# Performance work log

Hardware: AMD Instinct MI355X
Metric: run time of the kernel (lower is better)

The kernel has to match this reference:

```python
import jax, jax.numpy as jnp
import numpy as np


def setup_inputs() -> dict:
    key = jax.random.key(0)
    k1, k2 = jax.random.split(key)
    hw, bs, c = 16384, 16, 256
    nq = 100
    return {
        "query_feat": jax.random.normal(k1, (hw, bs, c), dtype=jnp.float32),
        "support_feat": jax.random.normal(k2, (nq, bs, c), dtype=jnp.float32),
        "h": 128,
        "w": 128,
    }


def reference(query_feat, support_feat, h, w):
    # query_feat: [hw, bs, c], support_feat: [nq, bs, c]
    hw, bs, c = query_feat.shape
    nq = support_feat.shape[0]
    dtype = query_feat.dtype

    side_normalizer = jnp.array([w, h], dtype=dtype)[None, None, :]  # [1,1,2]

    q = jnp.transpose(query_feat, (1, 0, 2))    # [bs, hw, c]
    s = jnp.transpose(support_feat, (1, 0, 2))  # [bs, nq, c]

    # bmm(q, s^T) -> [bs, hw, nq]; transpose -> [bs, nq, hw]
    similarity_flat = jnp.einsum('bnc,bkc->bnk', s, q)        # [bs, nq, hw]
    similarity = similarity_flat.reshape(bs, nq, h, w)

    # coordinate grid: stack([grid_x, grid_y]) with 'ij' meshgrid, flattened to [hw, 2]
    ys = jnp.linspace(0.5, h - 0.5, h, dtype=jnp.float32)
    xs = jnp.linspace(0.5, w - 0.5, w, dtype=jnp.float32)
    grid_y, grid_x = jnp.meshgrid(ys, xs, indexing='ij')      # [h, w] each
    coord = jnp.stack([grid_x, grid_y], axis=-1).reshape(hw, 2)  # [hw, 2]

    similarity_softmax = jax.nn.softmax(similarity_flat, axis=-1)  # [bs, nq, hw]

    proposal_for_loss = jnp.einsum('bnk,kd->bnd', similarity_softmax, coord) / side_normalizer

    # peak masking: argmax -> one_hot -> reshape (w, h) [faithful to original swap] -> 3x3 max pool
    max_pos = jnp.argmax(similarity_flat, axis=-1)            # [bs, nq]
    max_mask = jax.nn.one_hot(max_pos, hw, dtype=jnp.float32).reshape(bs, nq, w, h)
    local_max_mask = jax.lax.reduce_window(
        max_mask, -jnp.inf, jax.lax.max,
        window_dimensions=(1, 1, 3, 3), window_strides=(1, 1, 1, 1),
        padding=((0, 0), (0, 0), (1, 1), (1, 1)),
    ).reshape(bs, nq, hw)                                     # [bs, nq, hw]

    local_sm = similarity_softmax * local_max_mask            # [bs, nq, hw]
    local_sm = local_sm / (jnp.sum(local_sm, axis=-1, keepdims=True) + 1e-10)
    proposals = jnp.einsum('bnk,kd->bnd', local_sm, coord) / side_normalizer

    return (proposal_for_loss, similarity, proposals)
```

## Files before the change

kernel.cpp:

```cpp
#include <hip/hip_runtime.h>
#include <math.h>

#define HW   16384
#define BS   16
#define C    256
#define NQ   100
#define NQP  112
#define Hh   128
#define Ww   128

#define SIM_OFF   3200
#define PROPS_OFF (3200 + 26214400)

#define BM 256
#define BK 32
#define NBLK (HW / BM)

typedef _Float16 half8 __attribute__((ext_vector_type(8)));
typedef float f32x4 __attribute__((ext_vector_type(4)));

__device__ __forceinline__ void gll16(const void* gp, void* lp) {
    __builtin_amdgcn_global_load_lds((const __attribute__((address_space(1))) void*)gp,
                                     (__attribute__((address_space(3))) void*)lp, 16, 0, 0);
}

__device__ __forceinline__ void split8(const float4 a, const float4 b, half8& hi, half8& lo) {
    float f[8] = {a.x, a.y, a.z, a.w, b.x, b.y, b.z, b.w};
    _Float16 h[8], l[8];
    #pragma unroll
    for (int i = 0; i < 8; ++i) {
        h[i] = (_Float16)f[i];
        l[i] = (_Float16)(f[i] - (float)h[i]);
    }
    hi = *(half8*)h;
    lo = *(half8*)l;
}

__global__ __launch_bounds__(256) void split_S_kernel(const float* __restrict__ S,
                                                      _Float16* __restrict__ shi,
                                                      _Float16* __restrict__ slo)
{
    int idx4 = blockIdx.x * 256 + threadIdx.x;
    int idx = idx4 * 4;
    if (idx >= BS * NQP * C) return;
    int b = idx / (NQP * C);
    int rem = idx - b * (NQP * C);
    int n = rem / C;
    int k = rem - n * C;
    float4 v = make_float4(0.f, 0.f, 0.f, 0.f);
    if (n < NQ) v = *(const float4*)(S + ((size_t)n * BS + b) * C + k);
    _Float16 h[4], l[4];
    float f[4] = {v.x, v.y, v.z, v.w};
    #pragma unroll
    for (int i = 0; i < 4; ++i) {
        h[i] = (_Float16)f[i];
        l[i] = (_Float16)(f[i] - (float)h[i]);
    }
    *(uint2*)(shi + idx) = *(uint2*)h;
    *(uint2*)(slo + idx) = *(uint2*)l;
}

template<bool USE_WS>
__global__ __launch_bounds__(256, 2) void gemm_kernel(const float* __restrict__ Q,
                                                      const float* __restrict__ S,
                                                      const _Float16* __restrict__ ShiG,
                                                      const _Float16* __restrict__ SloG,
                                                      float* __restrict__ out,
                                                      float* __restrict__ pm,
                                                      float* __restrict__ pz,
                                                      float* __restrict__ pwx,
                                                      float* __restrict__ pwy,
                                                      int* __restrict__ pidx)
{
    __shared__ __align__(16) float    Qf[BM * BK];
    __shared__ __align__(16) _Float16 SHI[NQP * BK];
    __shared__ __align__(16) _Float16 SLO[NQP * BK];
    __shared__ __align__(16) float Ws[NQP][4][4];

    const int b    = blockIdx.y;
    const int hw0  = blockIdx.x * BM;
    const int t    = threadIdx.x;
    const int wid  = t >> 6;
    const int lane = t & 63;
    const int lr   = lane & 15;
    const int lg   = lane >> 4;

    f32x4 acc[4][7];
    #pragma unroll
    for (int am = 0; am < 4; ++am)
        #pragma unroll
        for (int bn = 0; bn < 7; ++bn)
            acc[am][bn] = (f32x4)(0.f);

    const int q_r8 = lane >> 3;
    const int q_gc = (lane & 7) ^ q_r8;
    const int s_r  = lane >> 2;
    const int s_gc = (lane & 3) ^ ((lane >> 3) & 3);

    for (int k0 = 0; k0 < C; k0 += BK) {
        #pragma unroll
        for (int p = 0; p < 8; ++p) {
            int rt = wid * 64 + p * 8;
            const float* g = Q + ((size_t)(hw0 + rt + q_r8) * BS + b) * C + k0 + q_gc * 4;
            gll16(g, &Qf[rt * BK]);
        }
        if (USE_WS) {
            for (int i = wid; i < 14; i += 4) {
                int r0 = (i % 7) * 16;
                _Float16* dst = (i < 7) ? &SHI[r0 * BK] : &SLO[r0 * BK];
                const _Float16* src = (i < 7) ? ShiG : SloG;
                const _Float16* g = src + ((size_t)b * NQP + r0 + s_r) * C + k0 + s_gc * 8;
                gll16(g, dst);
            }
        }
        __syncthreads();

        half8 qhi[4], qlo[4];
        #pragma unroll
        for (int am = 0; am < 4; ++am) {
            int row = wid * 64 + 16 * am + lr;
            int r7 = row & 7;
            float4 qa = *(const float4*)&Qf[row * BK + (((2 * lg + 0) ^ r7) << 2)];
            float4 qb = *(const float4*)&Qf[row * BK + (((2 * lg + 1) ^ r7) << 2)];
            split8(qa, qb, qhi[am], qlo[am]);
        }

        #pragma unroll
        for (int bn = 0; bn < 7; ++bn) {
            int row = 16 * bn + lr;
            half8 shi, slo;
            if (USE_WS) {
                int slot = lg ^ ((row >> 1) & 3);
                shi = *(const half8*)&SHI[row * BK + slot * 8];
                slo = *(const half8*)&SLO[row * BK + slot * 8];
            } else {
                if (row < NQ) {
                    const float* g = S + ((size_t)row * BS + b) * C + k0 + 8 * lg;
                    float4 sa = *(const float4*)g;
                    float4 sb = *(const float4*)(g + 4);
                    split8(sa, sb, shi, slo);
                } else {
                    shi = (half8)(_Float16)0.f;
                    slo = (half8)(_Float16)0.f;
                }
            }
            #pragma unroll
            for (int am = 0; am < 4; ++am) {
                acc[am][bn] = __builtin_amdgcn_mfma_f32_16x16x32_f16(qhi[am], shi, acc[am][bn], 0, 0, 0);
                acc[am][bn] = __builtin_amdgcn_mfma_f32_16x16x32_f16(qhi[am], slo, acc[am][bn], 0, 0, 0);
                acc[am][bn] = __builtin_amdgcn_mfma_f32_16x16x32_f16(qlo[am], shi, acc[am][bn], 0, 0, 0);
            }
        }
        __syncthreads();
    }

    float* simb = out + SIM_OFF;
    const int hwl0 = wid * 64 + 4 * lg;
    #pragma unroll
    for (int bn = 0; bn < 7; ++bn) {
        int nq = 16 * bn + lr;
        if (nq < NQ) {
            size_t rbase = ((size_t)(b * NQ + nq)) * HW + hw0 + hwl0;
            #pragma unroll
            for (int am = 0; am < 4; ++am)
                *(float4*)&simb[rbase + 16 * am] =
                    make_float4(acc[am][bn][0], acc[am][bn][1], acc[am][bn][2], acc[am][bn][3]);
        }
        if (USE_WS) {
            float vm = acc[0][bn][0];
            int   ci = hw0 + hwl0;
            #pragma unroll
            for (int am = 0; am < 4; ++am)
                #pragma unroll
                for (int j = 0; j < 4; ++j) {
                    float v = acc[am][bn][j];
                    if (v > vm) { vm = v; ci = hw0 + hwl0 + 16 * am + j; }
                }
            float z = 0.f, wx = 0.f;
            #pragma unroll
            for (int am = 0; am < 4; ++am)
                #pragma unroll
                for (int j = 0; j < 4; ++j) {
                    float e = __expf(acc[am][bn][j] - vm);
                    z += e;
                    wx += e * ((float)((hwl0 + 16 * am + j) & 127) + 0.5f);
                }
            #pragma unroll
            for (int off = 16; off < 64; off <<= 1) {
                float om = __shfl_xor(vm, off);
                int   oc = __shfl_xor(ci, off);
                float oz = __shfl_xor(z, off);
                float ox = __shfl_xor(wx, off);
                bool take = (om > vm) || (om == vm && oc < ci);
                float mn = take ? om : vm;
                float ss = __expf(vm - mn);
                float so = __expf(om - mn);
                z  = z * ss + oz * so;
                wx = wx * ss + ox * so;
                vm = mn;
                ci = take ? oc : ci;
            }
            if (lg == 0) {
                Ws[nq][wid][0] = vm;
                Ws[nq][wid][1] = __int_as_float(ci);
                Ws[nq][wid][2] = z;
                Ws[nq][wid][3] = wx;
            }
        }
    }
    if (USE_WS) {
        __syncthreads();
        if (t < NQ) {
            int nq = t;
            float M = -3.4e38f; int gi = 0;
            float mw[4], zw[4], xw[4]; int cw[4];
            #pragma unroll
            for (int w = 0; w < 4; ++w) {
                f32x4 tu = *(const f32x4*)&Ws[nq][w][0];
                mw[w] = tu[0]; cw[w] = __float_as_int(tu[1]); zw[w] = tu[2]; xw[w] = tu[3];
                if (mw[w] > M || (mw[w] == M && cw[w] < gi)) { M = mw[w]; gi = cw[w]; }
            }
            float ybase = (float)(hw0 >> 7) + 0.5f;
            float Zp = 0.f, WXp = 0.f, WYp = 0.f;
            #pragma unroll
            for (int w = 0; w < 4; ++w) {
                float s = __expf(mw[w] - M);
                Zp  += zw[w] * s;
                WXp += xw[w] * s;
                WYp += zw[w] * s * (ybase + (float)(w >> 1));
            }
            size_t pbase = ((size_t)b * NBLK + blockIdx.x) * NQ + nq;
            pm[pbase] = M; pz[pbase] = Zp; pwx[pbase] = WXp; pwy[pbase] = WYp;
            pidx[pbase] = gi;
        }
    }
}

__global__ __launch_bounds__(256) void finalize_kernel(const float* __restrict__ sim,
                                                       const float* __restrict__ pm,
                                                       const float* __restrict__ pz,
                                                       const float* __restrict__ pwx,
                                                       const float* __restrict__ pwy,
                                                       const int* __restrict__ pidx,
                                                       float* __restrict__ out)
{
    const int rglob = blockIdx.x * 4 + (threadIdx.x >> 6);
    const int lane  = threadIdx.x & 63;
    const int b     = rglob / NQ;
    const int n     = rglob - b * NQ;
    const size_t base = ((size_t)b * NBLK + lane) * NQ + n;

    float m  = pm[base];
    float z  = pz[base];
    float wx = pwx[base];
    float wy = pwy[base];
    int   gi = pidx[base];

    float v = m; int vi = gi;
    #pragma unroll
    for (int off = 1; off < 64; off <<= 1) {
        float ov = __shfl_xor(v, off);
        int   oi = __shfl_xor(vi, off);
        if (ov > v || (ov == v && oi < vi)) { v = ov; vi = oi; }
    }
    float s  = __expf(m - v);
    float Z  = z * s;
    float WX = wx * s;
    float WY = wy * s;
    #pragma unroll
    for (int off = 1; off < 64; off <<= 1) {
        Z  += __shfl_xor(Z, off);
        WX += __shfl_xor(WX, off);
        WY += __shfl_xor(WY, off);
    }
    if (lane == 0) {
        out[(size_t)rglob * 2 + 0] = (WX / Z) * (1.f / 128.f);
        out[(size_t)rglob * 2 + 1] = (WY / Z) * (1.f / 128.f);
        const float* srow = sim + (size_t)rglob * HW;
        int pr = vi >> 7, pc = vi & 127;
        float ls = 0.f, lx = 0.f, ly = 0.f;
        #pragma unroll
        for (int dr = -1; dr <= 1; ++dr) {
            #pragma unroll
            for (int dc = -1; dc <= 1; ++dc) {
                int r = pr + dr, c = pc + dc;
                if (r >= 0 && r < Ww && c >= 0 && c < Hh) {
                    int k = r * Hh + c;
                    float e = __expf(srow[k] - v);
                    ls += e;
                    lx += e * ((float)(k & 127) + 0.5f);
                    ly += e * ((float)(k >> 7) + 0.5f);
                }
            }
        }
        float denom = ls + 1e-10f * Z;
        out[PROPS_OFF + (size_t)rglob * 2 + 0] = (lx / denom) * (1.f / 128.f);
        out[PROPS_OFF + (size_t)rglob * 2 + 1] = (ly / denom) * (1.f / 128.f);
    }
}

__global__ __launch_bounds__(256) void reduce_kernel(const float* __restrict__ sim,
                                                     float* __restrict__ out)
{
    __shared__ float rowbuf[HW];
    __shared__ float s_pm[4];
    __shared__ int   s_pi[4];
    __shared__ float s_red[4][3];
    __shared__ float s_gmax;
    __shared__ int   s_gidx;

    const int row = blockIdx.x;
    const int t   = threadIdx.x;
    const int wid  = t >> 6;
    const int lane = t & 63;
    const float4* src4 = (const float4*)(sim + (size_t)row * HW);

    float vmax = -3.4e38f;
    int   vidx = 0;
    #pragma unroll
    for (int p = 0; p < 16; ++p) {
        int i4 = p * 256 + t;
        float4 v = src4[i4];
        *(float4*)&rowbuf[i4 * 4] = v;
        int base = i4 * 4;
        if (v.x > vmax) { vmax = v.x; vidx = base; }
        if (v.y > vmax) { vmax = v.y; vidx = base + 1; }
        if (v.z > vmax) { vmax = v.z; vidx = base + 2; }
        if (v.w > vmax) { vmax = v.w; vidx = base + 3; }
    }
    #pragma unroll
    for (int off = 32; off > 0; off >>= 1) {
        float ov = __shfl_down(vmax, off);
        int   oi = __shfl_down(vidx, off);
        if (ov > vmax || (ov == vmax && oi < vidx)) { vmax = ov; vidx = oi; }
    }
    if (lane == 0) { s_pm[wid] = vmax; s_pi[wid] = vidx; }
    __syncthreads();
    if (t == 0) {
        float gm = s_pm[0]; int gi = s_pi[0];
        #pragma unroll
        for (int wv = 1; wv < 4; ++wv) {
            float ov = s_pm[wv]; int oi = s_pi[wv];
            if (ov > gm || (ov == gm && oi < gi)) { gm = ov; gi = oi; }
        }
        s_gmax = gm; s_gidx = gi;
    }
    __syncthreads();
    const float gmax = s_gmax;

    float z = 0.f, wx = 0.f, wy = 0.f;
    #pragma unroll
    for (int p = 0; p < 16; ++p) {
        int i4 = p * 256 + t;
        float4 v = *(const float4*)&rowbuf[i4 * 4];
        int i = i4 * 4;
        float e0 = __expf(v.x - gmax), e1 = __expf(v.y - gmax);
        float e2 = __expf(v.z - gmax), e3 = __expf(v.w - gmax);
        z += (e0 + e1) + (e2 + e3);
        float cy = (float)(i >> 7) + 0.5f;
        float cx0 = (float)(i & (Ww - 1)) + 0.5f;
        wx += e0 * cx0 + e1 * (cx0 + 1.f) + e2 * (cx0 + 2.f) + e3 * (cx0 + 3.f);
        wy += (e0 + e1 + e2 + e3) * cy;
    }
    #pragma unroll
    for (int off = 32; off > 0; off >>= 1) {
        z  += __shfl_down(z, off);
        wx += __shfl_down(wx, off);
        wy += __shfl_down(wy, off);
    }
    if (lane == 0) { s_red[wid][0] = z; s_red[wid][1] = wx; s_red[wid][2] = wy; }
    __syncthreads();

    if (t == 0) {
        float Z = 0.f, WX = 0.f, WY = 0.f;
        #pragma unroll
        for (int wv = 0; wv < 4; ++wv) { Z += s_red[wv][0]; WX += s_red[wv][1]; WY += s_red[wv][2]; }

        out[(size_t)row * 2 + 0] = (WX / Z) * (1.0f / (float)Ww);
        out[(size_t)row * 2 + 1] = (WY / Z) * (1.0f / (float)Hh);

        int p  = s_gidx;
        int pr = p / Hh;
        int pc = p % Hh;
        float lsum = 0.f, lwx = 0.f, lwy = 0.f;
        #pragma unroll
        for (int di = -1; di <= 1; ++di) {
            #pragma unroll
            for (int dj = -1; dj <= 1; ++dj) {
                int r = pr + di, c = pc + dj;
                if (r >= 0 && r < Ww && c >= 0 && c < Hh) {
                    int k = r * Hh + c;
                    float e = __expf(rowbuf[k] - gmax);
                    lsum += e;
                    lwx  += e * ((float)(k & (Ww - 1)) + 0.5f);
                    lwy  += e * ((float)(k >> 7) + 0.5f);
                }
            }
        }
        float denom = lsum + 1e-10f * Z;
        out[PROPS_OFF + (size_t)row * 2 + 0] = (lwx / denom) * (1.0f / (float)Ww);
        out[PROPS_OFF + (size_t)row * 2 + 1] = (lwy / denom) * (1.0f / (float)Hh);
    }
}

extern "C" void kernel_launch(void* const* d_in, const int* in_sizes, int n_in,
                              void* d_out, int out_size, void* d_ws, size_t ws_size,
                              hipStream_t stream) {
    const float* Q = (const float*)d_in[0];
    const float* S = (const float*)d_in[1];
    float* out = (float*)d_out;

    const size_t splitElems = (size_t)BS * NQP * C;
    const size_t splitBytes = splitElems * 2 * sizeof(_Float16);
    const size_t nPart = (size_t)BS * NQ * NBLK;
    const size_t pOff  = (splitBytes + 255) & ~(size_t)255;
    const size_t wsNeeded = pOff + nPart * 5 * sizeof(float);

    if (ws_size >= wsNeeded) {
        _Float16* shi = (_Float16*)d_ws;
        _Float16* slo = shi + splitElems;
        float* pm  = (float*)((char*)d_ws + pOff);
        float* pz  = pm + nPart;
        float* pwx = pz + nPart;
        float* pwy = pwx + nPart;
        int*   pidx = (int*)(pwy + nPart);
        split_S_kernel<<<dim3((unsigned)((splitElems / 4 + 255) / 256)), 256, 0, stream>>>(S, shi, slo);
        gemm_kernel<true><<<dim3(HW / BM, BS), 256, 0, stream>>>(Q, S, shi, slo, out,
                                                                 pm, pz, pwx, pwy, pidx);
        finalize_kernel<<<dim3(BS * NQ / 4), 256, 0, stream>>>(out + SIM_OFF, pm, pz, pwx, pwy, pidx, out);
    } else {
        gemm_kernel<false><<<dim3(HW / BM, BS), 256, 0, stream>>>(Q, S, nullptr, nullptr, out,
                                                                  nullptr, nullptr, nullptr, nullptr, nullptr);
        reduce_kernel<<<dim3(BS * NQ), 256, 0, stream>>>(out + SIM_OFF, out);
    }
}
```

Baseline: 110.3 us.

## Halve GEMM tile rows, double-buffer Q staging, read split S directly from global

The GEMM tile shrinks from 256 to 128 rows per block with occupancy raised to 3, and Q tiles are double-buffered in LDS so the next K slice loads while MFMAs run. The per-step __syncthreads barriers are removed. The hi/lo split S operands are now read straight from global memory (L2/L1) instead of being staged in LDS. Since each block now covers exactly one image row, the y-weight partial is dropped and recomputed in finalize from the block index, which also handles two partials per lane. Risks include a possible race from removing the barriers between LDS writes and reads, more global traffic for S, and higher register pressure.

```diff
diff --git a/kernel.cpp b/kernel.cpp
--- a/kernel.cpp
+++ b/kernel.cpp
@@ -12,7 +12,7 @@
 #define SIM_OFF   3200
 #define PROPS_OFF (3200 + 26214400)
 
-#define BM 256
+#define BM 128
 #define BK 32
 #define NBLK (HW / BM)
 
@@ -61,7 +61,7 @@
 }
 
 template<bool USE_WS>
-__global__ __launch_bounds__(256, 2) void gemm_kernel(const float* __restrict__ Q,
+__global__ __launch_bounds__(256, 3) void gemm_kernel(const float* __restrict__ Q,
                                                       const float* __restrict__ S,
                                                       const _Float16* __restrict__ ShiG,
                                                       const _Float16* __restrict__ SloG,
@@ -69,12 +69,9 @@
                                                       float* __restrict__ pm,
                                                       float* __restrict__ pz,
                                                       float* __restrict__ pwx,
-                                                      float* __restrict__ pwy,
                                                       int* __restrict__ pidx)
 {
-    __shared__ __align__(16) float    Qf[BM * BK];
-    __shared__ __align__(16) _Float16 SHI[NQP * BK];
-    __shared__ __align__(16) _Float16 SLO[NQP * BK];
+    __shared__ __align__(16) float Qf[2][BM * BK];
     __shared__ __align__(16) float Ws[NQP][4][4];
 
     const int b    = blockIdx.y;
@@ -85,105 +82,105 @@
     const int lr   = lane & 15;
     const int lg   = lane >> 4;
 
-    f32x4 acc[4][7];
-    #pragma unroll
-    for (int am = 0; am < 4; ++am)
+    f32x4 acc[2][7];
+    #pragma unroll
+    for (int am = 0; am < 2; ++am)
         #pragma unroll
         for (int bn = 0; bn < 7; ++bn)
             acc[am][bn] = (f32x4)(0.f);
 
     const int q_r8 = lane >> 3;
     const int q_gc = (lane & 7) ^ q_r8;
-    const int s_r  = lane >> 2;
-    const int s_gc = (lane & 3) ^ ((lane >> 3) & 3);
-
-    for (int k0 = 0; k0 < C; k0 += BK) {
-        #pragma unroll
-        for (int p = 0; p < 8; ++p) {
-            int rt = wid * 64 + p * 8;
+
+    auto stageQ = [&](int buf, int k0) {
+        #pragma unroll
+        for (int p = 0; p < 4; ++p) {
+            int rt = wid * 32 + p * 8;
             const float* g = Q + ((size_t)(hw0 + rt + q_r8) * BS + b) * C + k0 + q_gc * 4;
-            gll16(g, &Qf[rt * BK]);
-        }
-        if (USE_WS) {
-            for (int i = wid; i < 14; i += 4) {
-                int r0 = (i % 7) * 16;
-                _Float16* dst = (i < 7) ? &SHI[r0 * BK] : &SLO[r0 * BK];
-                const _Float16* src = (i < 7) ? ShiG : SloG;
-                const _Float16* g = src + ((size_t)b * NQP + r0 + s_r) * C + k0 + s_gc * 8;
-                gll16(g, dst);
-            }
-        }
-        __syncthreads();
-
-        half8 qhi[4], qlo[4];
-        #pragma unroll
-        for (int am = 0; am < 4; ++am) {
-            int row = wid * 64 + 16 * am + lr;
+            gll16(g, &Qf[buf][rt * BK]);
+        }
+    };
+
+    stageQ(0, 0);
+    #pragma unroll 2
+    for (int step = 0; step < 8; ++step) {
+        const int k0  = step * BK;
+        const int cur = step & 1;
+
+        float4 qa[2], qb[2];
+        #pragma unroll
+        for (int am = 0; am < 2; ++am) {
+            int row = wid * 32 + 16 * am + lr;
             int r7 = row & 7;
-            float4 qa = *(const float4*)&Qf[row * BK + (((2 * lg + 0) ^ r7) << 2)];
-            float4 qb = *(const float4*)&Qf[row * BK + (((2 * lg + 1) ^ r7) << 2)];
-            split8(qa, qb, qhi[am], qlo[am]);
-        }
-
+            qa[am] = *(const float4*)&Qf[cur][row * BK + (((2 * lg + 0) ^ r7) << 2)];
+            qb[am] = *(const float4*)&Qf[cur][row * BK + (((2 * lg + 1) ^ r7) << 2)];
+        }
+
+        half8 shi[7], slo[7];
         #pragma unroll
         for (int bn = 0; bn < 7; ++bn) {
-            int row = 16 * bn + lr;
-            half8 shi, slo;
             if (USE_WS) {
-                int slot = lg ^ ((row >> 1) & 3);
-                shi = *(const half8*)&SHI[row * BK + slot * 8];
-                slo = *(const half8*)&SLO[row * BK + slot * 8];
+                size_t off = ((size_t)b * NQP + 16 * bn + lr) * C + k0 + 8 * lg;
+                shi[bn] = *(const half8*)(ShiG + off);
+                slo[bn] = *(const half8*)(SloG + off);
             } else {
+                int row = 16 * bn + lr;
                 if (row < NQ) {
                     const float* g = S + ((size_t)row * BS + b) * C + k0 + 8 * lg;
                     float4 sa = *(const float4*)g;
                     float4 sb = *(const float4*)(g + 4);
-                    split8(sa, sb, shi, slo);
+                    split8(sa, sb, shi[bn], slo[bn]);
                 } else {
-                    shi = (half8)(_Float16)0.f;
-                    slo = (half8)(_Float16)0.f;
+                    shi[bn] = (half8)(_Float16)0.f;
+                    slo[bn] = (half8)(_Float16)0.f;
                 }
             }
-            #pragma unroll
-            for (int am = 0; am < 4; ++am) {
-                acc[am][bn] = __builtin_amdgcn_mfma_f32_16x16x32_f16(qhi[am], shi, acc[am][bn], 0, 0, 0);
-                acc[am][bn] = __builtin_amdgcn_mfma_f32_16x16x32_f16(qhi[am], slo, acc[am][bn], 0, 0, 0);
-                acc[am][bn] = __builtin_amdgcn_mfma_f32_16x16x32_f16(qlo[am], shi, acc[am][bn], 0, 0, 0);
-            }
-        }
-        __syncthreads();
+        }
+
+        if (step < 7) stageQ(cur ^ 1, k0 + BK);
+
+        half8 qhi[2], qlo[2];
+        #pragma unroll
+        for (int am = 0; am < 2; ++am) split8(qa[am], qb[am], qhi[am], qlo[am]);
+
+        #pragma unroll
+        for (int bn = 0; bn < 7; ++bn)
+            #pragma unroll
+            for (int am = 0; am < 2; ++am) {
+                acc[am][bn] = __builtin_amdgcn_mfma_f32_16x16x32_f16(qhi[am], shi[bn], acc[am][bn], 0, 0, 0);
+                acc[am][bn] = __builtin_amdgcn_mfma_f32_16x16x32_f16(qhi[am], slo[bn], acc[am][bn], 0, 0, 0);
+                acc[am][bn] = __builtin_amdgcn_mfma_f32_16x16x32_f16(qlo[am], shi[bn], acc[am][bn], 0, 0, 0);
+            }
     }
 
     float* simb = out + SIM_OFF;
-    const int hwl0 = wid * 64 + 4 * lg;
+    const int hwl0 = wid * 32 + 4 * lg;
     #pragma unroll
     for (int bn = 0; bn < 7; ++bn) {
         int nq = 16 * bn + lr;
         if (nq < NQ) {
             size_t rbase = ((size_t)(b * NQ + nq)) * HW + hw0 + hwl0;
-            #pragma unroll
-            for (int am = 0; am < 4; ++am)
-                *(float4*)&simb[rbase + 16 * am] =
-                    make_float4(acc[am][bn][0], acc[am][bn][1], acc[am][bn][2], acc[am][bn][3]);
+            *(float4*)&simb[rbase]      = make_float4(acc[0][bn][0], acc[0][bn][1], acc[0][bn][2], acc[0][bn][3]);
+            *(float4*)&simb[rbase + 16] = make_float4(acc[1][bn][0], acc[1][bn][1], acc[1][bn][2], acc[1][bn][3]);
         }
         if (USE_WS) {
             float vm = acc[0][bn][0];
-            int   ci = hw0 + hwl0;
-            #pragma unroll
-            for (int am = 0; am < 4; ++am)
+            int   ci = hwl0;
+            #pragma unroll
+            for (int am = 0; am < 2; ++am)
                 #pragma unroll
                 for (int j = 0; j < 4; ++j) {
                     float v = acc[am][bn][j];
-                    if (v > vm) { vm = v; ci = hw0 + hwl0 + 16 * am + j; }
+                    if (v > vm) { vm = v; ci = hwl0 + 16 * am + j; }
                 }
             float z = 0.f, wx = 0.f;
             #pragma unroll
-            for (int am = 0; am < 4; ++am)
+            for (int am = 0; am < 2; ++am)
                 #pragma unroll
                 for (int j = 0; j < 4; ++j) {
                     float e = __expf(acc[am][bn][j] - vm);
                     z += e;
-                    wx += e * ((float)((hwl0 + 16 * am + j) & 127) + 0.5f);
+                    wx += e * ((float)(hwl0 + 16 * am + j) + 0.5f);
                 }
             #pragma unroll
             for (int off = 16; off < 64; off <<= 1) {
@@ -201,10 +198,8 @@
                 ci = take ? oc : ci;
             }
             if (lg == 0) {
-                Ws[nq][wid][0] = vm;
-                Ws[nq][wid][1] = __int_as_float(ci);
-                Ws[nq][wid][2] = z;
-                Ws[nq][wid][3] = wx;
+                f32x4 tu = {vm, __int_as_float(ci), z, wx};
+                *(f32x4*)&Ws[nq][wid][0] = tu;
             }
         }
     }
@@ -220,18 +215,16 @@
                 mw[w] = tu[0]; cw[w] = __float_as_int(tu[1]); zw[w] = tu[2]; xw[w] = tu[3];
                 if (mw[w] > M || (mw[w] == M && cw[w] < gi)) { M = mw[w]; gi = cw[w]; }
             }
-            float ybase = (float)(hw0 >> 7) + 0.5f;
-            float Zp = 0.f, WXp = 0.f, WYp = 0.f;
+            float Zp = 0.f, WXp = 0.f;
             #pragma unroll
             for (int w = 0; w < 4; ++w) {
                 float s = __expf(mw[w] - M);
                 Zp  += zw[w] * s;
                 WXp += xw[w] * s;
-                WYp += zw[w] * s * (ybase + (float)(w >> 1));
             }
             size_t pbase = ((size_t)b * NBLK + blockIdx.x) * NQ + nq;
-            pm[pbase] = M; pz[pbase] = Zp; pwx[pbase] = WXp; pwy[pbase] = WYp;
-            pidx[pbase] = gi;
+            pm[pbase] = M; pz[pbase] = Zp; pwx[pbase] = WXp;
+            pidx[pbase] = hw0 + gi;
         }
     }
 }
@@ -240,7 +233,6 @@
                                                        const float* __restrict__ pm,
                                                        const float* __restrict__ pz,
                                                        const float* __restrict__ pwx,
-                                                       const float* __restrict__ pwy,
                                                        const int* __restrict__ pidx,
                                                        float* __restrict__ out)
 {
@@ -248,25 +240,26 @@
     const int lane  = threadIdx.x & 63;
     const int b     = rglob / NQ;
     const int n     = rglob - b * NQ;
-    const size_t base = ((size_t)b * NBLK + lane) * NQ + n;
-
-    float m  = pm[base];
-    float z  = pz[base];
-    float wx = pwx[base];
-    float wy = pwy[base];
-    int   gi = pidx[base];
-
-    float v = m; int vi = gi;
+    const size_t b0 = ((size_t)b * NBLK + lane) * NQ + n;
+    const size_t b1 = ((size_t)b * NBLK + lane + 64) * NQ + n;
+
+    float m0 = pm[b0],   m1 = pm[b1];
+    float z0 = pz[b0],   z1 = pz[b1];
+    float x0 = pwx[b0],  x1 = pwx[b1];
+    int   i0 = pidx[b0], i1 = pidx[b1];
+
+    float v; int vi;
+    if (m0 >= m1) { v = m0; vi = i0; } else { v = m1; vi = i1; }
     #pragma unroll
     for (int off = 1; off < 64; off <<= 1) {
         float ov = __shfl_xor(v, off);
         int   oi = __shfl_xor(vi, off);
         if (ov > v || (ov == v && oi < vi)) { v = ov; vi = oi; }
     }
-    float s  = __expf(m - v);
-    float Z  = z * s;
-    float WX = wx * s;
-    float WY = wy * s;
+    float s0 = __expf(m0 - v), s1 = __expf(m1 - v);
+    float Z  = z0 * s0 + z1 * s1;
+    float WX = x0 * s0 + x1 * s1;
+    float WY = z0 * s0 * ((float)lane + 0.5f) + z1 * s1 * ((float)lane + 64.5f);
     #pragma unroll
     for (int off = 1; off < 64; off <<= 1) {
         Z  += __shfl_xor(Z, off);
@@ -414,7 +407,7 @@
     const size_t splitBytes = splitElems * 2 * sizeof(_Float16);
     const size_t nPart = (size_t)BS * NQ * NBLK;
     const size_t pOff  = (splitBytes + 255) & ~(size_t)255;
-    const size_t wsNeeded = pOff + nPart * 5 * sizeof(float);
+    const size_t wsNeeded = pOff + nPart * 4 * sizeof(float);
 
     if (ws_size >= wsNeeded) {
         _Float16* shi = (_Float16*)d_ws;
@@ -422,15 +415,14 @@
         float* pm  = (float*)((char*)d_ws + pOff);
         float* pz  = pm + nPart;
         float* pwx = pz + nPart;
-        float* pwy = pwx + nPart;
-        int*   pidx = (int*)(pwy + nPart);
+        int*   pidx = (int*)(pwx + nPart);
         split_S_kernel<<<dim3((unsigned)((splitElems / 4 + 255) / 256)), 256, 0, stream>>>(S, shi, slo);
         gemm_kernel<true><<<dim3(HW / BM, BS), 256, 0, stream>>>(Q, S, shi, slo, out,
-                                                                 pm, pz, pwx, pwy, pidx);
-        finalize_kernel<<<dim3(BS * NQ / 4), 256, 0, stream>>>(out + SIM_OFF, pm, pz, pwx, pwy, pidx, out);
+                                                                 pm, pz, pwx, pidx);
+        finalize_kernel<<<dim3(BS * NQ / 4), 256, 0, stream>>>(out + SIM_OFF, pm, pz, pwx, pidx, out);
     } else {
         gemm_kernel<false><<<dim3(HW / BM, BS), 256, 0, stream>>>(Q, S, nullptr, nullptr, out,
-                                                                  nullptr, nullptr, nullptr, nullptr, nullptr);
+                                                                  nullptr, nullptr, nullptr, nullptr);
         reduce_kernel<<<dim3(BS * NQ), 256, 0, stream>>>(out + SIM_OFF, out);
     }
 }
```

Measured after the change: 177.1 us. 60.6% more time.

## Double-buffer Q tiles in LDS and read split S directly from global

Applied to the files above, without the earlier changes.

The Q tile now uses two LDS buffers. The next k-slice is prefetched while the current slice is turned into MFMA operands, and both per-iteration block barriers are removed, since each wave only reads the rows it staged itself. The hi/lo fp16 parts of S are no longer staged through LDS; each lane loads them straight from global memory, relying on cache hits because S is small and shared across blocks. The within-block argmax index is kept relative and offset once at the end. The risk is correctness: without the barriers, the asynchronous LDS loads must be properly waited on before they are read, and the direct S loads add global-memory latency into the inner loop.

```diff
diff --git a/kernel.cpp b/kernel.cpp
--- a/kernel.cpp
+++ b/kernel.cpp
@@ -72,9 +72,7 @@
                                                       float* __restrict__ pwy,
                                                       int* __restrict__ pidx)
 {
-    __shared__ __align__(16) float    Qf[BM * BK];
-    __shared__ __align__(16) _Float16 SHI[NQP * BK];
-    __shared__ __align__(16) _Float16 SLO[NQP * BK];
+    __shared__ __align__(16) float Qf[2][BM * BK];
     __shared__ __align__(16) float Ws[NQP][4][4];
 
     const int b    = blockIdx.y;
@@ -94,64 +92,65 @@
 
     const int q_r8 = lane >> 3;
     const int q_gc = (lane & 7) ^ q_r8;
-    const int s_r  = lane >> 2;
-    const int s_gc = (lane & 3) ^ ((lane >> 3) & 3);
-
-    for (int k0 = 0; k0 < C; k0 += BK) {
+
+    auto stageQ = [&](int buf, int k0) {
         #pragma unroll
         for (int p = 0; p < 8; ++p) {
             int rt = wid * 64 + p * 8;
             const float* g = Q + ((size_t)(hw0 + rt + q_r8) * BS + b) * C + k0 + q_gc * 4;
-            gll16(g, &Qf[rt * BK]);
-        }
-        if (USE_WS) {
-            for (int i = wid; i < 14; i += 4) {
-                int r0 = (i % 7) * 16;
-                _Float16* dst = (i < 7) ? &SHI[r0 * BK] : &SLO[r0 * BK];
-                const _Float16* src = (i < 7) ? ShiG : SloG;
-                const _Float16* g = src + ((size_t)b * NQP + r0 + s_r) * C + k0 + s_gc * 8;
-                gll16(g, dst);
-            }
-        }
-        __syncthreads();
-
-        half8 qhi[4], qlo[4];
+            gll16(g, &Qf[buf][rt * BK]);
+        }
+    };
+
+    stageQ(0, 0);
+    for (int step = 0; step < 8; ++step) {
+        const int k0  = step * BK;
+        const int cur = step & 1;
+
+        float4 qa[4], qb[4];
         #pragma unroll
         for (int am = 0; am < 4; ++am) {
             int row = wid * 64 + 16 * am + lr;
             int r7 = row & 7;
-            float4 qa = *(const float4*)&Qf[row * BK + (((2 * lg + 0) ^ r7) << 2)];
-            float4 qb = *(const float4*)&Qf[row * BK + (((2 * lg + 1) ^ r7) << 2)];
-            split8(qa, qb, qhi[am], qlo[am]);
-        }
-
+            qa[am] = *(const float4*)&Qf[cur][row * BK + (((2 * lg + 0) ^ r7) << 2)];
+            qb[am] = *(const float4*)&Qf[cur][row * BK + (((2 * lg + 1) ^ r7) << 2)];
+        }
+
+        half8 shi[7], slo[7];
         #pragma unroll
         for (int bn = 0; bn < 7; ++bn) {
-            int row = 16 * bn + lr;
-            half8 shi, slo;
             if (USE_WS) {
-                int slot = lg ^ ((row >> 1) & 3);
-                shi = *(const half8*)&SHI[row * BK + slot * 8];
-                slo = *(const half8*)&SLO[row * BK + slot * 8];
+                size_t off = ((size_t)b * NQP + 16 * bn + lr) * C + k0 + 8 * lg;
+                shi[bn] = *(const half8*)(ShiG + off);
+                slo[bn] = *(const half8*)(SloG + off);
             } else {
+                int row = 16 * bn + lr;
                 if (row < NQ) {
                     const float* g = S + ((size_t)row * BS + b) * C + k0 + 8 * lg;
                     float4 sa = *(const float4*)g;
                     float4 sb = *(const float4*)(g + 4);
-                    split8(sa, sb, shi, slo);
+                    split8(sa, sb, shi[bn], slo[bn]);
                 } else {
-                    shi = (half8)(_Float16)0.f;
-                    slo = (half8)(_Float16)0.f;
+                    shi[bn] = (half8)(_Float16)0.f;
+                    slo[bn] = (half8)(_Float16)0.f;
                 }
             }
+        }
+
+        if (step < 7) stageQ(cur ^ 1, k0 + BK);
+
+        half8 qhi[4], qlo[4];
+        #pragma unroll
+        for (int am = 0; am < 4; ++am) split8(qa[am], qb[am], qhi[am], qlo[am]);
+
+        #pragma unroll
+        for (int bn = 0; bn < 7; ++bn)
             #pragma unroll
             for (int am = 0; am < 4; ++am) {
-                acc[am][bn] = __builtin_amdgcn_mfma_f32_16x16x32_f16(qhi[am], shi, acc[am][bn], 0, 0, 0);
-                acc[am][bn] = __builtin_amdgcn_mfma_f32_16x16x32_f16(qhi[am], slo, acc[am][bn], 0, 0, 0);
-                acc[am][bn] = __builtin_amdgcn_mfma_f32_16x16x32_f16(qlo[am], shi, acc[am][bn], 0, 0, 0);
-            }
-        }
-        __syncthreads();
+                acc[am][bn] = __builtin_amdgcn_mfma_f32_16x16x32_f16(qhi[am], shi[bn], acc[am][bn], 0, 0, 0);
+                acc[am][bn] = __builtin_amdgcn_mfma_f32_16x16x32_f16(qhi[am], slo[bn], acc[am][bn], 0, 0, 0);
+                acc[am][bn] = __builtin_amdgcn_mfma_f32_16x16x32_f16(qlo[am], shi[bn], acc[am][bn], 0, 0, 0);
+            }
     }
 
     float* simb = out + SIM_OFF;
@@ -168,13 +167,13 @@
         }
         if (USE_WS) {
             float vm = acc[0][bn][0];
-            int   ci = hw0 + hwl0;
+            int   ci = hwl0;
             #pragma unroll
             for (int am = 0; am < 4; ++am)
                 #pragma unroll
                 for (int j = 0; j < 4; ++j) {
                     float v = acc[am][bn][j];
-                    if (v > vm) { vm = v; ci = hw0 + hwl0 + 16 * am + j; }
+                    if (v > vm) { vm = v; ci = hwl0 + 16 * am + j; }
                 }
             float z = 0.f, wx = 0.f;
             #pragma unroll
@@ -201,10 +200,8 @@
                 ci = take ? oc : ci;
             }
             if (lg == 0) {
-                Ws[nq][wid][0] = vm;
-                Ws[nq][wid][1] = __int_as_float(ci);
-                Ws[nq][wid][2] = z;
-                Ws[nq][wid][3] = wx;
+                f32x4 tu = {vm, __int_as_float(ci), z, wx};
+                *(f32x4*)&Ws[nq][wid][0] = tu;
             }
         }
     }
@@ -231,7 +228,7 @@
             }
             size_t pbase = ((size_t)b * NBLK + blockIdx.x) * NQ + nq;
             pm[pbase] = M; pz[pbase] = Zp; pwx[pbase] = WXp; pwy[pbase] = WYp;
-            pidx[pbase] = gi;
+            pidx[pbase] = hw0 + gi;
         }
     }
 }
```

Result: slower. 128.2 us (+16.3%).
